# Kernel tuning notes

Measured on AMD Instinct MI355X. Metric: run time of the kernel, lower is better.

The kernel has to match this reference:

```python
import jax, jax.numpy as jnp
import numpy as np

N_L = 128
N_R = 128
VOCAB = 50000
IN_DIM = 512
MEM = 256
HID = 128
NCLS = 5


def _make_parents(n, seed):
    # children-before-parent topological order: parent[i] > i, root = n-1 with sentinel parent n
    rng = np.random.RandomState(seed)
    p = np.array([rng.randint(i + 1, n) if i < n - 1 else n for i in range(n)], dtype=np.int32)
    return jnp.asarray(p)


def setup_inputs() -> dict:
    key = jax.random.key(0)
    ks = jax.random.split(key, 18)
    s = 0.05
    inp = {
        'emb': jax.random.normal(ks[0], (VOCAB, IN_DIM), jnp.float32) * 0.1,
        'Wioux': jax.random.normal(ks[1], (IN_DIM, 3 * MEM), jnp.float32) * s,
        'bioux': jnp.zeros((3 * MEM,), jnp.float32),
        'Wiouh': jax.random.normal(ks[2], (MEM, 3 * MEM), jnp.float32) * s,
        'biouh': jnp.zeros((3 * MEM,), jnp.float32),
        'Wfx': jax.random.normal(ks[3], (IN_DIM, MEM), jnp.float32) * s,
        'bfx': jnp.zeros((MEM,), jnp.float32),
        'Wfh': jax.random.normal(ks[4], (MEM, MEM), jnp.float32) * s,
        'bfh': jnp.zeros((MEM,), jnp.float32),
        'Wattn': jax.random.normal(ks[5], (2 * MEM, MEM), jnp.float32) * s,
        'battn': jnp.zeros((MEM,), jnp.float32),
        'Wwh': jax.random.normal(ks[6], (2 * MEM, HID), jnp.float32) * s,
        'bwh': jnp.zeros((HID,), jnp.float32),
        'Wwp': jax.random.normal(ks[7], (HID, NCLS), jnp.float32) * s,
        'bwp': jnp.zeros((NCLS,), jnp.float32),
        'linputs': jax.random.randint(ks[8], (N_L,), 0, VOCAB, jnp.int32),
        'lparents': _make_parents(N_L, 11),
        'rinputs': jax.random.randint(ks[9], (N_R,), 0, VOCAB, jnp.int32),
        'rparents': _make_parents(N_R, 13),
    }
    return inp


def _tree_lstm(X, parents, Wioux, bioux, Wiouh, biouh, Wfx, bfx, Wfh, bfh):
    # X: [N, in_dim]; parents: [N] int, parent index > node index, root's parent == N (sentinel)
    N = X.shape[0]
    m = Wfh.shape[0]
    ioux_all = X @ Wioux + bioux          # [N, 3m] precomputed input contribution
    fx_all = X @ Wfx + bfx                # [N, m]
    fx_pad = jnp.concatenate([fx_all, jnp.zeros((1, m), X.dtype)], axis=0)  # sentinel row

    def step(carry, t):
        Hs, FCs, H = carry                # accumulators: sum of child h / forget-gated child c
        iou = ioux_all[t] + Hs[t] @ Wiouh + biouh
        i_, o_, u_ = jnp.split(iou, 3)
        i_ = jax.nn.sigmoid(i_)
        o_ = jax.nn.sigmoid(o_)
        u_ = jnp.tanh(u_)
        c = i_ * u_ + FCs[t]
        h = o_ * jnp.tanh(c)
        p = parents[t]
        f = jax.nn.sigmoid(h @ Wfh + bfh + fx_pad[p])  # forget gate of this child at its parent
        return (Hs.at[p].add(h), FCs.at[p].add(f * c), H.at[t].set(h)), None

    init = (jnp.zeros((N + 1, m), X.dtype), jnp.zeros((N + 1, m), X.dtype), jnp.zeros((N, m), X.dtype))
    (_, _, H), _ = jax.lax.scan(step, init, jnp.arange(N))
    return H


def reference(emb, Wioux, bioux, Wiouh, biouh, Wfx, bfx, Wfh, bfh,
              Wattn, battn, Wwh, bwh, Wwp, bwp,
              linputs, lparents, rinputs, rparents):
    Xl = emb[linputs]
    Xr = emb[rinputs]
    Hl = _tree_lstm(Xl, lparents, Wioux, bioux, Wiouh, biouh, Wfx, bfx, Wfh, bfh)  # [Nl, m]
    Hr = _tree_lstm(Xr, rparents, Wioux, bioux, Wiouh, biouh, Wfx, bfx, Wfh, bfh)  # [Nr, m]

    S = Hl @ Hr.T                                      # [Nl, Nr]
    beta_sum = jax.nn.softmax(S, axis=1) @ Hr          # [Nl, m]
    alpha_sum = jax.nn.softmax(S.T, axis=1) @ Hl       # [Nr, m]

    v_l = jnp.concatenate([Hl, beta_sum], axis=1) @ Wattn + battn
    v_r = jnp.concatenate([Hr, alpha_sum], axis=1) @ Wattn + battn

    lh = v_l[Hl.shape[0] - 1][None, :]                 # root of left tree
    rh = v_r[Hr.shape[0] - 1][None, :]                 # root of right tree

    vec = jnp.concatenate([lh * rh, jnp.abs(lh - rh)], axis=1)
    out = jax.nn.sigmoid(vec @ Wwh + bwh)
    return jax.nn.log_softmax(out @ Wwp + bwp, axis=1)
```

## Files before the change

kernel.cpp:

```cpp
#include <hip/hip_runtime.h>
#include <math.h>

typedef unsigned long long ull;

#define H_BYTE     0
#define IOUX_BYTE  262144
#define FLAG_BYTE  1310720

__device__ __forceinline__ float sigmf(float x){ return 1.0f/(1.0f+__expf(-x)); }
__device__ __forceinline__ float tanh_fast(float x){ float e=__expf(2.0f*x); return 1.0f-2.0f/(e+1.0f); }
__device__ __forceinline__ ull packf2(float lo, float hi){
    union{ float f[2]; ull u; } x; x.f[0]=lo; x.f[1]=hi; return x.u;
}
__device__ __forceinline__ ull aload64(const ull* p){
    return __hip_atomic_load(p, __ATOMIC_RELAXED, __HIP_MEMORY_SCOPE_AGENT);
}
__device__ __forceinline__ float aloadf(const float* p){
    return __hip_atomic_load(p, __ATOMIC_RELAXED, __HIP_MEMORY_SCOPE_AGENT);
}
__device__ __forceinline__ void astore64(ull* p, ull v){
    __hip_atomic_store(p, v, __ATOMIC_RELAXED, __HIP_MEMORY_SCOPE_AGENT);
}
__device__ __forceinline__ int aload32(const int* p){
    return __hip_atomic_load(p, __ATOMIC_RELAXED, __HIP_MEMORY_SCOPE_AGENT);
}
__device__ __forceinline__ void astore32(int* p, int v){
    __hip_atomic_store(p, v, __ATOMIC_RELAXED, __HIP_MEMORY_SCOPE_AGENT);
}

__device__ __forceinline__ void stage8(const ull* p0, const ull* p1, const ull* p2, const ull* p3,
                                       const ull* p4, const ull* p5, const ull* p6, const ull* p7,
                                       float4* r){
    asm volatile(
        "global_load_dwordx4 %0, %8, off sc0 sc1\n\t"
        "global_load_dwordx4 %1, %9, off sc0 sc1\n\t"
        "global_load_dwordx4 %2, %10, off sc0 sc1\n\t"
        "global_load_dwordx4 %3, %11, off sc0 sc1\n\t"
        "global_load_dwordx4 %4, %12, off sc0 sc1\n\t"
        "global_load_dwordx4 %5, %13, off sc0 sc1\n\t"
        "global_load_dwordx4 %6, %14, off sc0 sc1\n\t"
        "global_load_dwordx4 %7, %15, off sc0 sc1\n\t"
        "s_waitcnt vmcnt(0)"
        : "=&v"(r[0]), "=&v"(r[1]), "=&v"(r[2]), "=&v"(r[3]),
          "=&v"(r[4]), "=&v"(r[5]), "=&v"(r[6]), "=&v"(r[7])
        : "v"(p0), "v"(p1), "v"(p2), "v"(p3), "v"(p4), "v"(p5), "v"(p6), "v"(p7)
        : "memory");
    __builtin_amdgcn_sched_barrier(0);
}

__global__ __launch_bounds__(256) void k1_gemm(
        const float* __restrict__ emb,
        const float* __restrict__ Wioux, const float* __restrict__ bioux,
        const float* __restrict__ Wfx,   const float* __restrict__ bfx,
        const int* __restrict__ linputs, const int* __restrict__ rinputs,
        float* __restrict__ ws){
    int bid  = blockIdx.x;
    int tree = bid >> 6;
    int sub  = (bid >> 2) & 15;
    int q    = bid & 3;
    int n0   = q * 32;
    const int* inp = tree ? rinputs : linputs;
    float* dst = (float*)((char*)ws + IOUX_BYTE) + (size_t)(tree*16+sub)*128*64;

    __shared__ float Xs[32][513];
    __shared__ int toks[32];
    int tid = threadIdx.x;
    if (tid < 32) toks[tid] = inp[n0 + tid];
    __syncthreads();
    {
        int r = tid & 31, seg = tid >> 5;
        const float* src = emb + (size_t)toks[r]*512 + seg*64;
        #pragma unroll
        for (int ii = 0; ii < 16; ii++){
            float4 v = ((const float4*)src)[ii];
            Xs[r][seg*64 + ii*4 + 0] = v.x;
            Xs[r][seg*64 + ii*4 + 1] = v.y;
            Xs[r][seg*64 + ii*4 + 2] = v.z;
            Xs[r][seg*64 + ii*4 + 3] = v.w;
        }
    }
    __syncthreads();
    int c  = tid & 63;
    int ng = tid >> 6;
    int g = c >> 4, jj = c & 15;
    const float* Wcol; int ld; float bias;
    if (g < 3){ int col = g*256 + sub*16 + jj; Wcol = Wioux + col; ld = 768; bias = bioux[col]; }
    else      { int col = sub*16 + jj;         Wcol = Wfx + col;   ld = 256; bias = bfx[col]; }
    float acc[8] = {0,0,0,0,0,0,0,0};
    #pragma unroll 4
    for (int k = 0; k < 512; k++){
        float w = Wcol[(size_t)k*ld];
        #pragma unroll
        for (int i = 0; i < 8; i++) acc[i] = fmaf(Xs[ng*8+i][k], w, acc[i]);
    }
    #pragma unroll
    for (int i = 0; i < 8; i++)
        dst[(size_t)(n0 + ng*8 + i)*64 + c] = acc[i] + bias;
}

__global__ __launch_bounds__(256, 1) void k2_scan(
        const float* __restrict__ Wiouh, const float* __restrict__ biouh,
        const float* __restrict__ Wfh,   const float* __restrict__ bfh,
        const int* __restrict__ lparents, const int* __restrict__ rparents,
        const float* __restrict__ Wattn, const float* __restrict__ battn,
        const float* __restrict__ Wwh,   const float* __restrict__ bwh,
        const float* __restrict__ Wwp,   const float* __restrict__ bwp,
        float* __restrict__ ws, float* __restrict__ out){

    int bid = blockIdx.x;
    int tree = bid >> 4;
    int sub  = bid & 15;
    int slice = sub * 16;
    const int* parents = tree ? rparents : lparents;

    ull* H2all = (ull*)((char*)ws + H_BYTE);
    ull* H2 = H2all + (size_t)tree*128*128;
    const float* iosrc = (const float*)((char*)ws + IOUX_BYTE) + (size_t)(tree*16+sub)*128*64;
    int* flagB = (int*)((char*)ws + FLAG_BYTE);
    int* prog  = flagB + tree*16;
    int* fin   = flagB + 32;

    __shared__ float hv[32][320];
    __shared__ float hsin[16][321];
    __shared__ float red[4][48][17];
    __shared__ float FCtmp[32][17];
    __shared__ float fcin[16][17];
    __shared__ float cc[128][17];
    __shared__ float ioufL[128][68];
    __shared__ int par[128], rnd[128], order[128], kids[128], posOf[128];
    __shared__ int rstart[129], kstart[129], cnt[129];
    __shared__ int clist[128], cpar[128];
    __shared__ int coff[17];
    __shared__ int changed, maxPosS;

    int tid = threadIdx.x;
    int a = tid >> 4;
    int j = tid & 15;
    int jcol = slice + j;

    float Wi[16], Wo[16], Wu[16], Wf[16];
    #pragma unroll
    for (int kk = 0; kk < 16; kk++){
        int k = a*16 + kk;
        Wi[kk] = Wiouh[(size_t)k*768 + jcol];
        Wo[kk] = Wiouh[(size_t)k*768 + 256 + jcol];
        Wu[kk] = Wiouh[(size_t)k*768 + 512 + jcol];
        Wf[kk] = Wfh[(size_t)k*256 + jcol];
    }
    float bioI = biouh[jcol], bioO = biouh[256+jcol], bioU = biouh[512+jcol];
    float bfv  = bfh[jcol];

    for (int i = tid; i < 128*16; i += 256){
        int n = i >> 4, f4 = i & 15;
        float4 v = ((const float4*)(iosrc + (size_t)n*64))[f4];
        int c0 = f4*4;
        ioufL[n][c0+0]=v.x; ioufL[n][c0+1]=v.y; ioufL[n][c0+2]=v.z; ioufL[n][c0+3]=v.w;
    }

    if (tid < 128){ par[tid] = parents[tid]; rnd[tid] = 0; }
    __syncthreads();
    for(;;){
        if (tid==0) changed = 0;
        __syncthreads();
        if (tid < 128){
            int p = par[tid];
            if (p < 128){
                int v = rnd[tid] + 1;
                if (atomicMax(&rnd[p], v) < v) changed = 1;
            }
        }
        __syncthreads();
        int done = (changed == 0);
        __syncthreads();
        if (done) break;
    }
    int nr = rnd[127] + 1;

    if (tid <= 128) cnt[tid] = 0;
    __syncthreads();
    if (tid < 128) atomicAdd(&cnt[rnd[tid]], 1);
    __syncthreads();
    if (tid==0){ int s2=0; for(int r2=0;r2<128;r2++){ rstart[r2]=s2; s2+=cnt[r2]; } rstart[128]=s2; }
    __syncthreads();
    if (tid < 128){
        int r2 = rnd[tid], rk = 0;
        for (int t2 = 0; t2 < tid; t2++) rk += (rnd[t2]==r2);
        int pos = rstart[r2]+rk;
        order[pos] = tid;
        posOf[tid] = pos;
    }
    __syncthreads();
    if (tid <= 128) cnt[tid] = 0;
    __syncthreads();
    if (tid < 128) atomicAdd(&cnt[par[tid]], 1);
    __syncthreads();
    if (tid==0){ int s2=0; for(int t2=0;t2<=128;t2++){ kstart[t2]=s2; s2+=cnt[t2]; } }
    __syncthreads();
    if (tid < 128){
        int p = par[tid], rk = 0;
        for (int t2 = 0; t2 < tid; t2++) rk += (par[t2]==p);
        kids[kstart[p]+rk] = tid;
    }
    __syncthreads();

    {
        int rs = rstart[0], re = rstart[1];
        for (int b0 = rs; b0 < re; b0 += 16){
            int t = (b0 + a < re) ? order[b0 + a] : -1;
            float h = 0.f;
            if (t >= 0){
                float iv = ioufL[t][j]    + bioI;
                float ov = ioufL[t][16+j] + bioO;
                float uv = ioufL[t][32+j] + bioU;
                float cv = sigmf(iv) * tanh_fast(uv);
                h = sigmf(ov) * tanh_fast(cv);
                cc[t][j] = cv;
            }
            float hp = __shfl_xor(h, 1);
            if (t >= 0 && (j & 1) == 0)
                astore64(&H2[(size_t)t*128 + (slice>>1) + (j>>1)], packf2(h, hp));
            __syncthreads();
            if (tid == 0){
                int done = b0 + 16 < re ? b0 + 16 : re;
                astore32(&prog[sub], done);
            }
        }
    }

    for (int r = 1; r < nr; r++){
        int rs = rstart[r], re = rstart[r+1];
        for (int b0 = rs; b0 < re; b0 += 16){
            int nn = re - b0; if (nn > 16) nn = 16;
            for (int i = tid; i < 16*321; i += 256) (&hsin[0][0])[i] = 0.f;
            fcin[a][j] = 0.f;
            if (tid == 0){
                maxPosS = 0;
                int s2 = 0;
                for (int i2 = 0; i2 < 16; i2++){
                    coff[i2] = s2;
                    if (i2 < nn){ int t2 = order[b0+i2]; s2 += kstart[t2+1]-kstart[t2]; }
                }
                coff[16] = s2;
            }
            __syncthreads();
            if (tid < nn){
                int t2 = order[b0+tid];
                int o = coff[tid];
                for (int ci = kstart[t2]; ci < kstart[t2+1]; ci++, o++){
                    clist[o] = kids[ci]; cpar[o] = t2;
                }
            }
            __syncthreads();
            int M = coff[16];
            if (tid < M) atomicMax(&maxPosS, posOf[clist[tid]]);
            __syncthreads();

            if (tid < 64){
                int need = maxPosS + 1;
                for(;;){
                    int v = (tid < 16) ? aload32(&prog[tid]) : 0x7fffffff;
                    if (__all((tid < 16) ? (v >= need) : 1)) break;
                    __builtin_amdgcn_s_sleep(2);
                }
            }
            __syncthreads();

            for (int cb = 0; cb < M; cb += 32){
                int mm = M - cb; if (mm > 32) mm = 32;
                {
                    int c16 = tid & 63;
                    int rw  = tid >> 6;
                    int k0 = c16 * 4;
                    int km = (k0 >> 4)*20 + (k0 & 15);
                    const ull* base = H2;
                    const ull* pp[8];
                    #pragma unroll
                    for (int p = 0; p < 8; p++){
                        int s = p*4 + rw;
                        int idx = (s < mm) ? clist[cb+s] : clist[cb];
                        pp[p] = base + (size_t)idx*128 + c16*2;
                    }
                    float4 rr[8];
                    stage8(pp[0],pp[1],pp[2],pp[3],pp[4],pp[5],pp[6],pp[7], rr);
                    #pragma unroll
                    for (int p = 0; p < 8; p++){
                        int s = p*4 + rw;
                        if (s < mm) *(float4*)&hv[s][km] = rr[p];
                    }
                }
                __syncthreads();
                for (int s = 0; s < mm; s++){
                    const float* row = &hv[s][a*20];
                    float acc2 = 0.f;
                    #pragma unroll
                    for (int kk = 0; kk < 16; kk++) acc2 = fmaf(Wf[kk], row[kk], acc2);
                    acc2 += __shfl_xor(acc2, 16);
                    acc2 += __shfl_xor(acc2, 32);
                    if ((a & 3) == 0) red[tid>>6][s][j] = acc2;
                }
                __syncthreads();
                for (int pass = 0; pass*16 < mm; pass++){
                    int s = pass*16 + a;
                    if (s < mm){
                        int o = cb + s;
                        float sf = red[0][s][j]+red[1][s][j]+red[2][s][j]+red[3][s][j];
                        float f = sigmf(sf + bfv + ioufL[cpar[o]][48+j]);
                        FCtmp[s][j] = f * cc[clist[o]][j];
                    }
                }
                __syncthreads();
                {
                    int o0 = coff[a]   > cb    ? coff[a]   : cb;
                    int o1 = coff[a+1] < cb+mm ? coff[a+1] : cb+mm;
                    float* dst = &hsin[a][j*20];
                    float fa = 0.f;
                    for (int o = o0; o < o1; o++){
                        int s = o - cb;
                        const float* src = &hv[s][j*20];
                        #pragma unroll
                        for (int kk = 0; kk < 16; kk++) dst[kk] += src[kk];
                        fa += FCtmp[s][j];
                    }
                    fcin[a][j] += fa;
                }
                __syncthreads();
            }

            for (int n = 0; n < nn; n++){
                const float* row = &hsin[n][a*20];
                float x=0.f, y=0.f, z=0.f;
                #pragma unroll
                for (int kk = 0; kk < 16; kk++){
                    float v = row[kk];
                    x = fmaf(Wi[kk], v, x);
                    y = fmaf(Wo[kk], v, y);
                    z = fmaf(Wu[kk], v, z);
                }
                x += __shfl_xor(x,16); x += __shfl_xor(x,32);
                y += __shfl_xor(y,16); y += __shfl_xor(y,32);
                z += __shfl_xor(z,16); z += __shfl_xor(z,32);
                if ((a & 3) == 0){
                    int w = tid >> 6;
                    red[w][n][j]    = x;
                    red[w][16+n][j] = y;
                    red[w][32+n][j] = z;
                }
            }
            __syncthreads();
            {
                int t = (a < nn) ? order[b0+a] : -1;
                float h = 0.f;
                if (t >= 0){
                    float si = red[0][a][j]+red[1][a][j]+red[2][a][j]+red[3][a][j];
                    float so = red[0][16+a][j]+red[1][16+a][j]+red[2][16+a][j]+red[3][16+a][j];
                    float su = red[0][32+a][j]+red[1][32+a][j]+red[2][32+a][j]+red[3][32+a][j];
                    float iv = si + ioufL[t][j]    + bioI;
                    float ov = so + ioufL[t][16+j] + bioO;
                    float uv = su + ioufL[t][32+j] + bioU;
                    float cv = fmaf(sigmf(iv), tanh_fast(uv), fcin[a][j]);
                    h = sigmf(ov) * tanh_fast(cv);
                    cc[t][j] = cv;
                }
                float hp = __shfl_xor(h, 1);
                if (t >= 0 && (j & 1) == 0)
                    astore64(&H2[(size_t)t*128 + (slice>>1) + (j>>1)], packf2(h, hp));
            }
            __syncthreads();
            if (tid == 0) astore32(&prog[sub], b0 + nn);
        }
    }

    if (tid == 0) astore32(&fin[bid], 1);
    if (bid != 0) return;
    if (tid < 64){
        for(;;){
            int v = (tid < 32) ? aload32(&fin[tid]) : 1;
            if (__all((tid < 32) ? (v == 1) : 1)) break;
            __builtin_amdgcn_s_sleep(2);
        }
    }
    __syncthreads();

    float* F  = &hv[0][0];
    float* rl = F,        *rr  = F + 256;
    float* sA = F + 512,  *sB  = F + 640;
    float* bet= F + 768,  *alp = F + 1024;
    float* vl = F + 1280, *vr  = F + 1536;
    float* vec= F + 1792, *hid = F + 2304;
    const ull* HuL = H2all;
    const ull* HuR = H2all + (size_t)128*128;

    {
        union{ ull u; float f[2]; } w2;
        if (tid < 128){
            w2.u = aload64(&HuL[(size_t)127*128 + tid]);
            rl[2*tid] = w2.f[0]; rl[2*tid+1] = w2.f[1];
        } else {
            int p = tid - 128;
            w2.u = aload64(&HuR[(size_t)127*128 + p]);
            rr[2*p] = w2.f[0]; rr[2*p+1] = w2.f[1];
        }
    }
    __syncthreads();
    {
        int i = tid & 127;
        const ull* row = (tid < 128) ? &HuR[(size_t)i*128] : &HuL[(size_t)i*128];
        const float* rt = (tid < 128) ? rl : rr;
        float acc2 = 0.f;
        for (int p0 = 0; p0 < 128; p0 += 16){
            ull u[16];
            #pragma unroll
            for (int q2 = 0; q2 < 16; q2++) u[q2] = aload64(&row[p0+q2]);
            #pragma unroll
            for (int q2 = 0; q2 < 16; q2++){
                union{ ull uu; float f[2]; } w2; w2.uu = u[q2];
                acc2 = fmaf(w2.f[0], rt[2*(p0+q2)],   acc2);
                acc2 = fmaf(w2.f[1], rt[2*(p0+q2)+1], acc2);
            }
        }
        if (tid < 128) sA[i] = acc2; else sB[i] = acc2;
    }
    __syncthreads();
    if (tid < 2){
        float* v = tid ? sB : sA;
        float m = -1e30f;
        for (int k = 0; k < 128; k++) m = fmaxf(m, v[k]);
        float su2 = 0.f;
        for (int k = 0; k < 128; k++){ float e = __expf(v[k]-m); v[k]=e; su2+=e; }
        float inv = 1.0f/su2;
        for (int k = 0; k < 128; k++) v[k] *= inv;
    }
    __syncthreads();
    {
        const float* HrF = (const float*)HuR;
        const float* HlF = (const float*)HuL;
        float b = 0.f, al = 0.f;
        for (int i0 = 0; i0 < 128; i0 += 16){
            float ur[16], ulv[16];
            #pragma unroll
            for (int q2 = 0; q2 < 16; q2++){
                ur[q2]  = aloadf(&HrF[(size_t)(i0+q2)*256 + tid]);
                ulv[q2] = aloadf(&HlF[(size_t)(i0+q2)*256 + tid]);
            }
            #pragma unroll
            for (int q2 = 0; q2 < 16; q2++){
                b  = fmaf(sA[i0+q2], ur[q2],  b);
                al = fmaf(sB[i0+q2], ulv[q2], al);
            }
        }
        bet[tid] = b; alp[tid] = al;
    }
    __syncthreads();
    {
        float x = 0.f, y = 0.f;
        for (int k = 0; k < 256; k++){
            float w = Wattn[(size_t)k*256 + tid];
            x = fmaf(rl[k], w, x);
            y = fmaf(rr[k], w, y);
        }
        for (int k = 0; k < 256; k++){
            float w = Wattn[(size_t)(256+k)*256 + tid];
            x = fmaf(bet[k], w, x);
            y = fmaf(alp[k], w, y);
        }
        vl[tid] = x + battn[tid];
        vr[tid] = y + battn[tid];
    }
    __syncthreads();
    vec[tid]     = vl[tid]*vr[tid];
    vec[256+tid] = fabsf(vl[tid]-vr[tid]);
    __syncthreads();
    if (tid < 128){
        float acc2 = 0.f;
        for (int k = 0; k < 512; k++) acc2 = fmaf(vec[k], Wwh[(size_t)k*128+tid], acc2);
        hid[tid] = sigmf(acc2 + bwh[tid]);
    }
    __syncthreads();
    if (tid == 0){
        float lg[5];
        for (int c2 = 0; c2 < 5; c2++){
            float acc2 = bwp[c2];
            for (int k = 0; k < 128; k++) acc2 = fmaf(hid[k], Wwp[k*5+c2], acc2);
            lg[c2] = acc2;
        }
        float m = lg[0];
        for (int c2 = 1; c2 < 5; c2++) m = fmaxf(m, lg[c2]);
        float su2 = 0.f;
        for (int c2 = 0; c2 < 5; c2++) su2 += __expf(lg[c2]-m);
        float ls = logf(su2);
        for (int c2 = 0; c2 < 5; c2++) out[c2] = lg[c2]-m-ls;
    }
}

extern "C" void kernel_launch(void* const* d_in, const int* in_sizes, int n_in,
                              void* d_out, int out_size, void* d_ws, size_t ws_size,
                              hipStream_t stream) {
    const float* emb    = (const float*)d_in[0];
    const float* Wioux  = (const float*)d_in[1];
    const float* bioux  = (const float*)d_in[2];
    const float* Wiouh  = (const float*)d_in[3];
    const float* biouh  = (const float*)d_in[4];
    const float* Wfx    = (const float*)d_in[5];
    const float* bfx    = (const float*)d_in[6];
    const float* Wfh    = (const float*)d_in[7];
    const float* bfh    = (const float*)d_in[8];
    const float* Wattn  = (const float*)d_in[9];
    const float* battn  = (const float*)d_in[10];
    const float* Wwh    = (const float*)d_in[11];
    const float* bwh    = (const float*)d_in[12];
    const float* Wwp    = (const float*)d_in[13];
    const float* bwp    = (const float*)d_in[14];
    const int* linputs  = (const int*)d_in[15];
    const int* lparents = (const int*)d_in[16];
    const int* rinputs  = (const int*)d_in[17];
    const int* rparents = (const int*)d_in[18];
    float* ws  = (float*)d_ws;
    float* out = (float*)d_out;

    hipMemsetAsync((char*)d_ws + FLAG_BYTE, 0, 256, stream);
    k1_gemm<<<128, 256, 0, stream>>>(emb, Wioux, bioux, Wfx, bfx,
                                     linputs, rinputs, ws);
    k2_scan<<<32, 256, 0, stream>>>(Wiouh, biouh, Wfh, bfh, lparents, rparents,
                                    Wattn, battn, Wwh, bwh, Wwp, bwp, ws, out);
}
```

Baseline: 187.8 us.

## Precompute tree batch schedule and remap threads to cut per-step barriers

Builds the per-batch child lists and offsets for all scan steps once, before the recurrence, instead of rebuilding them serially inside each step. Thread mapping moves from (node, column) to (column, k-group), so the gate dot-product reductions finish inside a wavefront with xor shuffles and no longer go through a shared reduction buffer and its extra barriers. The cross-block wait becomes a level-based check that caches the last seen progress, and the hsin zero-fill is replaced by first-write assignment. The cost is more shuffle work per step, fully unrolled loops over 16 and 32 rows, and added register pressure.

```diff
diff --git a/kernel.cpp b/kernel.cpp
--- a/kernel.cpp
+++ b/kernel.cpp
@@ -98,6 +98,8 @@
         dst[(size_t)(n0 + ng*8 + i)*64 + c] = acc[i] + bias;
 }
 
+#define MAXB 136
+
 __global__ __launch_bounds__(256, 1) void k2_scan(
         const float* __restrict__ Wiouh, const float* __restrict__ biouh,
         const float* __restrict__ Wfh,   const float* __restrict__ bfh,
@@ -120,28 +122,28 @@
     int* prog  = flagB + tree*16;
     int* fin   = flagB + 32;
 
-    __shared__ float hv[32][320];
-    __shared__ float hsin[16][321];
-    __shared__ float red[4][48][17];
+    __shared__ float hv[32][324];
+    __shared__ float hsin[16][324];
     __shared__ float FCtmp[32][17];
-    __shared__ float fcin[16][17];
     __shared__ float cc[128][17];
     __shared__ float ioufL[128][68];
-    __shared__ int par[128], rnd[128], order[128], kids[128], posOf[128];
+    __shared__ int par[128], rnd[128], order[128], kids[128], rankOf[128], posOf[128];
     __shared__ int rstart[129], kstart[129], cnt[129];
-    __shared__ int clist[128], cpar[128];
-    __shared__ int coff[17];
-    __shared__ int changed, maxPosS;
+    __shared__ int bStart[MAXB], bN[MAXB], bM[MAXB], bCbase[MAXB], bLevel[MAXB];
+    __shared__ int bFirst[128];
+    __shared__ int sCoff[MAXB][17];
+    __shared__ int sClist[128];
+    __shared__ int changed, nbS;
 
     int tid = threadIdx.x;
-    int a = tid >> 4;
-    int j = tid & 15;
-    int jcol = slice + j;
+    int cj = tid >> 4;
+    int kg = tid & 15;
+    int jcol = slice + cj;
 
     float Wi[16], Wo[16], Wu[16], Wf[16];
     #pragma unroll
     for (int kk = 0; kk < 16; kk++){
-        int k = a*16 + kk;
+        int k = kg*16 + kk;
         Wi[kk] = Wiouh[(size_t)k*768 + jcol];
         Wo[kk] = Wiouh[(size_t)k*768 + 256 + jcol];
         Wu[kk] = Wiouh[(size_t)k*768 + 512 + jcol];
@@ -200,85 +202,93 @@
         int p = par[tid], rk = 0;
         for (int t2 = 0; t2 < tid; t2++) rk += (par[t2]==p);
         kids[kstart[p]+rk] = tid;
-    }
-    __syncthreads();
-
-    {
-        int rs = rstart[0], re = rstart[1];
-        for (int b0 = rs; b0 < re; b0 += 16){
-            int t = (b0 + a < re) ? order[b0 + a] : -1;
-            float h = 0.f;
+        rankOf[tid] = rk;
+    }
+    __syncthreads();
+
+    if (tid == 0){
+        int nb = 0;
+        for (int r = 0; r < nr; r++){
+            bFirst[r] = nb;
+            for (int b0 = rstart[r]; b0 < rstart[r+1]; b0 += 16){
+                int nn = rstart[r+1] - b0; if (nn > 16) nn = 16;
+                bStart[nb] = b0; bN[nb] = nn; bLevel[nb] = r; nb++;
+            }
+        }
+        nbS = nb;
+    }
+    __syncthreads();
+    int NB = nbS;
+    if (tid < NB){
+        int base = 0;
+        for (int s = 0; s < 16; s++){
+            sCoff[tid][s] = base;
+            if (s < bN[tid]){
+                int t = order[bStart[tid] + s];
+                base += kstart[t+1] - kstart[t];
+            }
+        }
+        sCoff[tid][16] = base;
+        bM[tid] = base;
+    }
+    __syncthreads();
+    if (tid == 0){ int acc = 0; for (int b = 0; b < NB; b++){ bCbase[b] = acc; acc += bM[b]; } }
+    __syncthreads();
+    if (tid < 128){
+        int p = par[tid];
+        if (p < 128){
+            int rp = rnd[p];
+            int idx = posOf[p] - rstart[rp];
+            int bb = bFirst[rp] + (idx >> 4);
+            int sp = idx & 15;
+            sClist[bCbase[bb] + sCoff[bb][sp] + rankOf[tid]] = tid;
+        }
+    }
+    __syncthreads();
+
+    int seenV = 0;
+    for (int b = 0; b < NB; b++){
+        int lev = bLevel[b];
+        int n0 = bStart[b], nn = bN[b];
+        int t = (kg < nn) ? order[n0 + kg] : -1;
+        float h = 0.f;
+
+        if (lev == 0){
             if (t >= 0){
-                float iv = ioufL[t][j]    + bioI;
-                float ov = ioufL[t][16+j] + bioO;
-                float uv = ioufL[t][32+j] + bioU;
+                float iv = ioufL[t][cj]    + bioI;
+                float ov = ioufL[t][16+cj] + bioO;
+                float uv = ioufL[t][32+cj] + bioU;
                 float cv = sigmf(iv) * tanh_fast(uv);
                 h = sigmf(ov) * tanh_fast(cv);
-                cc[t][j] = cv;
-            }
-            float hp = __shfl_xor(h, 1);
-            if (t >= 0 && (j & 1) == 0)
-                astore64(&H2[(size_t)t*128 + (slice>>1) + (j>>1)], packf2(h, hp));
+                cc[t][cj] = cv;
+            }
+        } else {
+            int need = rstart[lev];
+            if (tid < 16 && seenV < need){
+                for(;;){
+                    seenV = aload32(&prog[tid]);
+                    if (seenV >= need) break;
+                    __builtin_amdgcn_s_sleep(1);
+                }
+            }
             __syncthreads();
-            if (tid == 0){
-                int done = b0 + 16 < re ? b0 + 16 : re;
-                astore32(&prog[sub], done);
-            }
-        }
-    }
-
-    for (int r = 1; r < nr; r++){
-        int rs = rstart[r], re = rstart[r+1];
-        for (int b0 = rs; b0 < re; b0 += 16){
-            int nn = re - b0; if (nn > 16) nn = 16;
-            for (int i = tid; i < 16*321; i += 256) (&hsin[0][0])[i] = 0.f;
-            fcin[a][j] = 0.f;
-            if (tid == 0){
-                maxPosS = 0;
-                int s2 = 0;
-                for (int i2 = 0; i2 < 16; i2++){
-                    coff[i2] = s2;
-                    if (i2 < nn){ int t2 = order[b0+i2]; s2 += kstart[t2+1]-kstart[t2]; }
-                }
-                coff[16] = s2;
-            }
-            __syncthreads();
-            if (tid < nn){
-                int t2 = order[b0+tid];
-                int o = coff[tid];
-                for (int ci = kstart[t2]; ci < kstart[t2+1]; ci++, o++){
-                    clist[o] = kids[ci]; cpar[o] = t2;
-                }
-            }
-            __syncthreads();
-            int M = coff[16];
-            if (tid < M) atomicMax(&maxPosS, posOf[clist[tid]]);
-            __syncthreads();
-
-            if (tid < 64){
-                int need = maxPosS + 1;
-                for(;;){
-                    int v = (tid < 16) ? aload32(&prog[tid]) : 0x7fffffff;
-                    if (__all((tid < 16) ? (v >= need) : 1)) break;
-                    __builtin_amdgcn_s_sleep(2);
-                }
-            }
-            __syncthreads();
+
+            int M = bM[b], cbase = bCbase[b];
+            int o0 = sCoff[b][kg], o1 = sCoff[b][kg+1];
+            float fc = 0.f;
+            bool first = true;
 
             for (int cb = 0; cb < M; cb += 32){
                 int mm = M - cb; if (mm > 32) mm = 32;
                 {
-                    int c16 = tid & 63;
-                    int rw  = tid >> 6;
-                    int k0 = c16 * 4;
-                    int km = (k0 >> 4)*20 + (k0 & 15);
-                    const ull* base = H2;
+                    int c16 = tid & 63, rw = tid >> 6;
+                    int k0 = c16*4, km = (k0>>4)*20 + (k0&15);
                     const ull* pp[8];
                     #pragma unroll
                     for (int p = 0; p < 8; p++){
                         int s = p*4 + rw;
-                        int idx = (s < mm) ? clist[cb+s] : clist[cb];
-                        pp[p] = base + (size_t)idx*128 + c16*2;
+                        int idx = (s < mm) ? sClist[cbase+cb+s] : sClist[cbase+cb];
+                        pp[p] = H2 + (size_t)idx*128 + c16*2;
                     }
                     float4 rr[8];
                     stage8(pp[0],pp[1],pp[2],pp[3],pp[4],pp[5],pp[6],pp[7], rr);
@@ -289,46 +299,64 @@
                     }
                 }
                 __syncthreads();
-                for (int s = 0; s < mm; s++){
-                    const float* row = &hv[s][a*20];
-                    float acc2 = 0.f;
-                    #pragma unroll
-                    for (int kk = 0; kk < 16; kk++) acc2 = fmaf(Wf[kk], row[kk], acc2);
-                    acc2 += __shfl_xor(acc2, 16);
-                    acc2 += __shfl_xor(acc2, 32);
-                    if ((a & 3) == 0) red[tid>>6][s][j] = acc2;
+
+                float fs0 = 0.f, fs1 = 0.f;
+                #pragma unroll
+                for (int s = 0; s < 32; s++){
+                    if (s < mm){
+                        const float* row = &hv[s][kg*20];
+                        float acc2 = 0.f;
+                        #pragma unroll
+                        for (int kk = 0; kk < 16; kk++) acc2 = fmaf(Wf[kk], row[kk], acc2);
+                        acc2 += __shfl_xor(acc2, 1);
+                        acc2 += __shfl_xor(acc2, 2);
+                        acc2 += __shfl_xor(acc2, 4);
+                        acc2 += __shfl_xor(acc2, 8);
+                        if (kg == (s & 15)){ if (s < 16) fs0 = acc2; else fs1 = acc2; }
+                    }
                 }
-                __syncthreads();
-                for (int pass = 0; pass*16 < mm; pass++){
-                    int s = pass*16 + a;
+                {
+                    int s = kg;
                     if (s < mm){
-                        int o = cb + s;
-                        float sf = red[0][s][j]+red[1][s][j]+red[2][s][j]+red[3][s][j];
-                        float f = sigmf(sf + bfv + ioufL[cpar[o]][48+j]);
-                        FCtmp[s][j] = f * cc[clist[o]][j];
+                        int c = sClist[cbase+cb+s]; int p = par[c];
+                        float f = sigmf(fs0 + bfv + ioufL[p][48+cj]);
+                        FCtmp[s][cj] = f * cc[c][cj];
+                    }
+                    s = kg + 16;
+                    if (s < mm){
+                        int c = sClist[cbase+cb+s]; int p = par[c];
+                        float f = sigmf(fs1 + bfv + ioufL[p][48+cj]);
+                        FCtmp[s][cj] = f * cc[c][cj];
                     }
                 }
                 __syncthreads();
+
                 {
-                    int o0 = coff[a]   > cb    ? coff[a]   : cb;
-                    int o1 = coff[a+1] < cb+mm ? coff[a+1] : cb+mm;
-                    float* dst = &hsin[a][j*20];
-                    float fa = 0.f;
-                    for (int o = o0; o < o1; o++){
+                    int a0 = o0 > cb ? o0 : cb;
+                    int a1 = o1 < cb+mm ? o1 : cb+mm;
+                    float* dst = &hsin[kg][cj*20];
+                    for (int o = a0; o < a1; o++){
                         int s = o - cb;
-                        const float* src = &hv[s][j*20];
-                        #pragma unroll
-                        for (int kk = 0; kk < 16; kk++) dst[kk] += src[kk];
-                        fa += FCtmp[s][j];
+                        const float* src = &hv[s][cj*20];
+                        if (first){
+                            #pragma unroll
+                            for (int kk = 0; kk < 16; kk++) dst[kk] = src[kk];
+                            first = false;
+                        } else {
+                            #pragma unroll
+                            for (int kk = 0; kk < 16; kk++) dst[kk] += src[kk];
+                        }
+                        fc += FCtmp[s][cj];
                     }
-                    fcin[a][j] += fa;
                 }
                 __syncthreads();
             }
 
-            for (int n = 0; n < nn; n++){
-                const float* row = &hsin[n][a*20];
-                float x=0.f, y=0.f, z=0.f;
+            float gx = 0.f, gy = 0.f, gz = 0.f;
+            #pragma unroll
+            for (int n = 0; n < 16; n++){
+                const float* row = &hsin[n][kg*20];
+                float x = 0.f, y = 0.f, z = 0.f;
                 #pragma unroll
                 for (int kk = 0; kk < 16; kk++){
                     float v = row[kk];
@@ -336,38 +364,26 @@
                     y = fmaf(Wo[kk], v, y);
                     z = fmaf(Wu[kk], v, z);
                 }
-                x += __shfl_xor(x,16); x += __shfl_xor(x,32);
-                y += __shfl_xor(y,16); y += __shfl_xor(y,32);
-                z += __shfl_xor(z,16); z += __shfl_xor(z,32);
-                if ((a & 3) == 0){
-                    int w = tid >> 6;
-                    red[w][n][j]    = x;
-                    red[w][16+n][j] = y;
-                    red[w][32+n][j] = z;
-                }
-            }
-            __syncthreads();
-            {
-                int t = (a < nn) ? order[b0+a] : -1;
-                float h = 0.f;
-                if (t >= 0){
-                    float si = red[0][a][j]+red[1][a][j]+red[2][a][j]+red[3][a][j];
-                    float so = red[0][16+a][j]+red[1][16+a][j]+red[2][16+a][j]+red[3][16+a][j];
-                    float su = red[0][32+a][j]+red[1][32+a][j]+red[2][32+a][j]+red[3][32+a][j];
-                    float iv = si + ioufL[t][j]    + bioI;
-                    float ov = so + ioufL[t][16+j] + bioO;
-                    float uv = su + ioufL[t][32+j] + bioU;
-                    float cv = fmaf(sigmf(iv), tanh_fast(uv), fcin[a][j]);
-                    h = sigmf(ov) * tanh_fast(cv);
-                    cc[t][j] = cv;
-                }
-                float hp = __shfl_xor(h, 1);
-                if (t >= 0 && (j & 1) == 0)
-                    astore64(&H2[(size_t)t*128 + (slice>>1) + (j>>1)], packf2(h, hp));
-            }
-            __syncthreads();
-            if (tid == 0) astore32(&prog[sub], b0 + nn);
-        }
+                x += __shfl_xor(x,1); x += __shfl_xor(x,2); x += __shfl_xor(x,4); x += __shfl_xor(x,8);
+                y += __shfl_xor(y,1); y += __shfl_xor(y,2); y += __shfl_xor(y,4); y += __shfl_xor(y,8);
+                z += __shfl_xor(z,1); z += __shfl_xor(z,2); z += __shfl_xor(z,4); z += __shfl_xor(z,8);
+                if (kg == n){ gx = x; gy = y; gz = z; }
+            }
+            if (t >= 0){
+                float iv = gx + ioufL[t][cj]    + bioI;
+                float ov = gy + ioufL[t][16+cj] + bioO;
+                float uv = gz + ioufL[t][32+cj] + bioU;
+                float cv = fmaf(sigmf(iv), tanh_fast(uv), fc);
+                h = sigmf(ov) * tanh_fast(cv);
+                cc[t][cj] = cv;
+            }
+        }
+
+        float hp = __shfl_xor(h, 16);
+        if (t >= 0 && (cj & 1) == 0)
+            astore64(&H2[(size_t)t*128 + (slice>>1) + (cj>>1)], packf2(h, hp));
+        __syncthreads();
+        if (tid == 0) astore32(&prog[sub], n0 + nn);
     }
 
     if (tid == 0) astore32(&fin[bid], 1);
```

Result: slower. 228.0 us (+21.4%).

## Replace progress-counter barriers with sentinel-poisoned H buffer polling

Applied to the files above, without the earlier changes.

The first kernel now fills the H workspace with an all-ones NaN sentinel. The recurrent kernel drops the per-slice progress counters and the max-position spin wait, and instead re-polls each child's H row until no word still holds the sentinel. This removes the global flag round trips and the extra block barriers per batch, so consumers wait only on the data they actually need. In exchange, every staged load is validated and may be retried, and correctness depends on the init kernel finishing first and on a computed h never having the sentinel bit pattern.

```diff
diff --git a/kernel.cpp b/kernel.cpp
--- a/kernel.cpp
+++ b/kernel.cpp
@@ -55,6 +55,12 @@
         const int* __restrict__ linputs, const int* __restrict__ rinputs,
         float* __restrict__ ws){
     int bid  = blockIdx.x;
+    int tid = threadIdx.x;
+    {
+        ull* Hc = (ull*)((char*)ws + H_BYTE) + (size_t)bid*256;
+        Hc[tid] = ~0ull;
+        if (tid < 0) return;
+    }
     int tree = bid >> 6;
     int sub  = (bid >> 2) & 15;
     int q    = bid & 3;
@@ -64,7 +70,6 @@
 
     __shared__ float Xs[32][513];
     __shared__ int toks[32];
-    int tid = threadIdx.x;
     if (tid < 32) toks[tid] = inp[n0 + tid];
     __syncthreads();
     {
@@ -117,7 +122,6 @@
     ull* H2 = H2all + (size_t)tree*128*128;
     const float* iosrc = (const float*)((char*)ws + IOUX_BYTE) + (size_t)(tree*16+sub)*128*64;
     int* flagB = (int*)((char*)ws + FLAG_BYTE);
-    int* prog  = flagB + tree*16;
     int* fin   = flagB + 32;
 
     __shared__ float hv[32][320];
@@ -127,11 +131,11 @@
     __shared__ float fcin[16][17];
     __shared__ float cc[128][17];
     __shared__ float ioufL[128][68];
-    __shared__ int par[128], rnd[128], order[128], kids[128], posOf[128];
+    __shared__ int par[128], rnd[128], order[128], kids[128];
     __shared__ int rstart[129], kstart[129], cnt[129];
     __shared__ int clist[128], cpar[128];
     __shared__ int coff[17];
-    __shared__ int changed, maxPosS;
+    __shared__ int changed;
 
     int tid = threadIdx.x;
     int a = tid >> 4;
@@ -185,9 +189,7 @@
     if (tid < 128){
         int r2 = rnd[tid], rk = 0;
         for (int t2 = 0; t2 < tid; t2++) rk += (rnd[t2]==r2);
-        int pos = rstart[r2]+rk;
-        order[pos] = tid;
-        posOf[tid] = pos;
+        order[rstart[r2]+rk] = tid;
     }
     __syncthreads();
     if (tid <= 128) cnt[tid] = 0;
@@ -219,11 +221,6 @@
             float hp = __shfl_xor(h, 1);
             if (t >= 0 && (j & 1) == 0)
                 astore64(&H2[(size_t)t*128 + (slice>>1) + (j>>1)], packf2(h, hp));
-            __syncthreads();
-            if (tid == 0){
-                int done = b0 + 16 < re ? b0 + 16 : re;
-                astore32(&prog[sub], done);
-            }
         }
     }
 
@@ -234,7 +231,6 @@
             for (int i = tid; i < 16*321; i += 256) (&hsin[0][0])[i] = 0.f;
             fcin[a][j] = 0.f;
             if (tid == 0){
-                maxPosS = 0;
                 int s2 = 0;
                 for (int i2 = 0; i2 < 16; i2++){
                     coff[i2] = s2;
@@ -252,18 +248,6 @@
             }
             __syncthreads();
             int M = coff[16];
-            if (tid < M) atomicMax(&maxPosS, posOf[clist[tid]]);
-            __syncthreads();
-
-            if (tid < 64){
-                int need = maxPosS + 1;
-                for(;;){
-                    int v = (tid < 16) ? aload32(&prog[tid]) : 0x7fffffff;
-                    if (__all((tid < 16) ? (v >= need) : 1)) break;
-                    __builtin_amdgcn_s_sleep(2);
-                }
-            }
-            __syncthreads();
 
             for (int cb = 0; cb < M; cb += 32){
                 int mm = M - cb; if (mm > 32) mm = 32;
@@ -272,16 +256,29 @@
                     int rw  = tid >> 6;
                     int k0 = c16 * 4;
                     int km = (k0 >> 4)*20 + (k0 & 15);
-                    const ull* base = H2;
                     const ull* pp[8];
                     #pragma unroll
                     for (int p = 0; p < 8; p++){
                         int s = p*4 + rw;
                         int idx = (s < mm) ? clist[cb+s] : clist[cb];
-                        pp[p] = base + (size_t)idx*128 + c16*2;
+                        pp[p] = H2 + (size_t)idx*128 + c16*2;
                     }
                     float4 rr[8];
-                    stage8(pp[0],pp[1],pp[2],pp[3],pp[4],pp[5],pp[6],pp[7], rr);
+                    for(;;){
+                        stage8(pp[0],pp[1],pp[2],pp[3],pp[4],pp[5],pp[6],pp[7], rr);
+                        bool ok = true;
+                        #pragma unroll
+                        for (int p = 0; p < 8; p++){
+                            int s = p*4 + rw;
+                            if (s < mm){
+                                uint4 u = *(uint4*)&rr[p];
+                                ok = ok && (u.x != 0xFFFFFFFFu) && (u.y != 0xFFFFFFFFu)
+                                        && (u.z != 0xFFFFFFFFu) && (u.w != 0xFFFFFFFFu);
+                            }
+                        }
+                        if (ok) break;
+                        __builtin_amdgcn_s_sleep(1);
+                    }
                     #pragma unroll
                     for (int p = 0; p < 8; p++){
                         int s = p*4 + rw;
@@ -366,7 +363,6 @@
                     astore64(&H2[(size_t)t*128 + (slice>>1) + (j>>1)], packf2(h, hp));
             }
             __syncthreads();
-            if (tid == 0) astore32(&prog[sub], b0 + nn);
         }
     }
 
```

Result: faster. 178.7 us (-4.9%).
